# Performance work log

Hardware: AMD Instinct MI355X
Metric: run time of the kernel (lower is better)

The kernel has to match this reference:

```python
import jax, jax.numpy as jnp
import numpy as np

D_MODEL = 1024
N_HEADS = 16
D_HEAD = D_MODEL // N_HEADS


def setup_inputs() -> dict:
    key = jax.random.key(0)
    k_x, k_wqkv, k_bqkv, k_wout, k_bout = jax.random.split(key, 5)
    x = jax.random.normal(k_x, (4, 2048, D_MODEL), dtype=jnp.float32)
    s = 1.0 / np.sqrt(D_MODEL)
    W_qkv = jax.random.uniform(k_wqkv, (D_MODEL, 3 * D_MODEL), jnp.float32, -s, s)
    b_qkv = jax.random.uniform(k_bqkv, (3 * D_MODEL,), jnp.float32, -s, s)
    W_out = jax.random.uniform(k_wout, (D_MODEL, D_MODEL), jnp.float32, -s, s)
    b_out = jax.random.uniform(k_bout, (D_MODEL,), jnp.float32, -s, s)
    return {"x": x, "W_qkv": W_qkv, "b_qkv": b_qkv, "W_out": W_out, "b_out": b_out}


def reference(x, W_qkv, b_qkv, W_out, b_out):
    B, S, _ = x.shape
    qkv = x @ W_qkv + b_qkv                      # [B,S,3*d_model]
    qkv = qkv.reshape(B, S, N_HEADS, 3 * D_HEAD).transpose(0, 2, 1, 3)  # [B,H,S,3*dh]
    q, k, v = jnp.split(qkv, 3, axis=-1)          # each [B,H,S,dh]
    scale = 1.0 / jnp.sqrt(jnp.asarray(D_HEAD, x.dtype))
    scores = jnp.einsum("bhqd,bhkd->bhqk", q, k) * scale  # [B,H,S,S]
    attn_weights = jax.nn.softmax(scores, axis=-1)
    attn = jnp.einsum("bhqk,bhkd->bhqd", attn_weights, v)  # [B,H,S,dh]
    attn = attn.transpose(0, 2, 1, 3).reshape(B, S, D_MODEL)
    return attn @ W_out + b_out
```

## Files before the change

kernel.cpp:

```cpp
#include <hip/hip_runtime.h>

typedef unsigned short u16;
typedef __bf16 bf16x8 __attribute__((ext_vector_type(8)));
typedef __bf16 bf16x4 __attribute__((ext_vector_type(4)));
typedef short s16x4 __attribute__((ext_vector_type(4)));
typedef float f32x4 __attribute__((ext_vector_type(4)));

union U4B8 { uint4 u; bf16x8 v; u16 s[8]; };
union U2S4 { uint2 u2; s16x4 s; bf16x4 h; };

__device__ __forceinline__ u16 f2b(float f) {
  union { float f; unsigned u; } x; x.f = f;
  unsigned u = x.u + 0x7fffu + ((x.u >> 16) & 1u);
  return (u16)(u >> 16);
}

__global__ __launch_bounds__(256) void cvt_f32_bf16(const float* __restrict__ in,
                                                    u16* __restrict__ out) {
  int i = blockIdx.x * 256 + threadIdx.x;
  float4 v = ((const float4*)in)[i];
  ushort4 h;
  h.x = f2b(v.x); h.y = f2b(v.y); h.z = f2b(v.z); h.w = f2b(v.w);
  ((ushort4*)out)[i] = h;
}

__global__ __launch_bounds__(256) void transpose_w(const float* __restrict__ in,
                                                   u16* __restrict__ out, int K, int N) {
  __shared__ u16 t[64 * 72];
  int k0 = blockIdx.y * 64, n0 = blockIdx.x * 64;
  int tid = threadIdx.x;
#pragma unroll
  for (int p = 0; p < 4; ++p) {
    int idx = p * 256 + tid;
    int k = idx >> 4, ng = idx & 15;
    float4 v = *(const float4*)(in + (k0 + k) * N + n0 + ng * 4);
    t[(ng * 4 + 0) * 72 + k] = f2b(v.x);
    t[(ng * 4 + 1) * 72 + k] = f2b(v.y);
    t[(ng * 4 + 2) * 72 + k] = f2b(v.z);
    t[(ng * 4 + 3) * 72 + k] = f2b(v.w);
  }
  __syncthreads();
#pragma unroll
  for (int p = 0; p < 2; ++p) {
    int idx = p * 256 + tid;
    int n = idx >> 3, kg = (idx & 7) * 8;
    uint4 u = *(uint4*)(&t[n * 72 + kg]);
    *(uint4*)(out + (n0 + n) * K + k0 + kg) = u;
  }
}

template <int MODE>
__global__ __launch_bounds__(256) void gemm_bf16(const u16* __restrict__ A,
                                                 const u16* __restrict__ B,
                                                 const float* __restrict__ bias,
                                                 float* __restrict__ outf,
                                                 u16* __restrict__ Qo, u16* __restrict__ Ko,
                                                 u16* __restrict__ Vo) {
  __shared__ u16 a_lds[128 * 32];
  __shared__ u16 b_lds[128 * 32];
  int tid = threadIdx.x;
  int l = tid & 63, w = tid >> 6;
  int wr = (w >> 1) * 64, wc = (w & 1) * 64;
  int m0 = blockIdx.y * 128, n0 = blockIdx.x * 128;
  int r15 = l & 15;
  int ka = (l >> 4) * 8;
  int r0 = tid >> 2, kg0 = (tid & 3) * 8;
  f32x4 acc[4][4] = {};
  for (int kt = 0; kt < 32; ++kt) {
    int k0 = kt * 32;
    __syncthreads();
    __builtin_amdgcn_global_load_lds(
        (const __attribute__((address_space(1))) void*)(A + (m0 + r0) * 1024 + k0 + kg0),
        (__attribute__((address_space(3))) void*)(&a_lds[tid * 8]), 16, 0, 0);
    __builtin_amdgcn_global_load_lds(
        (const __attribute__((address_space(1))) void*)(A + (m0 + 64 + r0) * 1024 + k0 + kg0),
        (__attribute__((address_space(3))) void*)(&a_lds[2048 + tid * 8]), 16, 0, 0);
    __builtin_amdgcn_global_load_lds(
        (const __attribute__((address_space(1))) void*)(B + (n0 + r0) * 1024 + k0 + kg0),
        (__attribute__((address_space(3))) void*)(&b_lds[tid * 8]), 16, 0, 0);
    __builtin_amdgcn_global_load_lds(
        (const __attribute__((address_space(1))) void*)(B + (n0 + 64 + r0) * 1024 + k0 + kg0),
        (__attribute__((address_space(3))) void*)(&b_lds[2048 + tid * 8]), 16, 0, 0);
    __syncthreads();
    bf16x8 af[4], bf[4];
#pragma unroll
    for (int i = 0; i < 4; ++i) {
      U4B8 ua; ua.u = *(uint4*)(&a_lds[(wr + i * 16 + r15) * 32 + ka]); af[i] = ua.v;
      U4B8 ub; ub.u = *(uint4*)(&b_lds[(wc + i * 16 + r15) * 32 + ka]); bf[i] = ub.v;
    }
#pragma unroll
    for (int i = 0; i < 4; ++i)
#pragma unroll
      for (int j = 0; j < 4; ++j)
        acc[i][j] = __builtin_amdgcn_mfma_f32_16x16x32_bf16(af[i], bf[j], acc[i][j], 0, 0, 0);
  }
  int rbase = (l >> 4) * 4;
#pragma unroll
  for (int i = 0; i < 4; ++i)
#pragma unroll
    for (int j = 0; j < 4; ++j) {
      int n = n0 + wc + j * 16 + r15;
      float bv = bias[n];
#pragma unroll
      for (int r = 0; r < 4; ++r) {
        int m = m0 + wr + i * 16 + rbase + r;
        float val = acc[i][j][r] + bv;
        if (MODE == 0) {
          int h = n / 192, rem = n % 192;
          int part = rem >> 6, d = rem & 63;
          int b = m >> 11, s = m & 2047;
          int off = (((b * 16 + h) * 2048) + s) * 64 + d;
          u16 hv = f2b(part == 0 ? val * 0.180336880111f : val);
          if (part == 0) Qo[off] = hv;
          else if (part == 1) Ko[off] = hv;
          else Vo[off] = hv;
        } else {
          outf[m * 1024 + n] = val;
        }
      }
    }
}

__global__ __launch_bounds__(512, 2) void attn_fwd(const u16* __restrict__ Q,
                                                   const u16* __restrict__ K,
                                                   const u16* __restrict__ V,
                                                   u16* __restrict__ O) {
  __shared__ u16 lds[16384];
  int tid = threadIdx.x;
  int l = tid & 63, w = tid >> 6;
  int g = l >> 4, r15 = l & 15, r7 = r15 & 7;
  int bid = blockIdx.x;
  int qb = (bid >> 3) & 7;
  int bh = (bid & 7) * 8 + (bid >> 6);
  const u16* Kb = K + bh * 131072;
  const u16* Vb = V + bh * 131072;
  int ka = g * 8;
  int qbase = qb * 256 + w * 32;
  U4B8 t0, t1, t2, t3;
  t0.u = *(const uint4*)(Q + bh * 131072 + (qbase + r15) * 64 + ka);
  t1.u = *(const uint4*)(Q + bh * 131072 + (qbase + r15) * 64 + 32 + ka);
  t2.u = *(const uint4*)(Q + bh * 131072 + (qbase + 16 + r15) * 64 + ka);
  t3.u = *(const uint4*)(Q + bh * 131072 + (qbase + 16 + r15) * 64 + 32 + ka);
  bf16x8 qf00 = t0.v, qf01 = t1.v, qf10 = t2.v, qf11 = t3.v;

  int kaddr[4];
#pragma unroll
  for (int c = 0; c < 4; ++c) kaddr[c] = (c * 16 + r15) * 64 + ((g ^ r7) << 3);
  int vaddr0[4];
#pragma unroll
  for (int dq = 0; dq < 4; ++dq) {
    int d = r15 + 16 * dq;
    int vsw = ((d >> 3) ^ d) & 15;
    vaddr0[dq] = 8192 + d * 64 + ((g ^ vsw) << 2);
  }

  int krow0 = tid >> 3;
  int kcg = (((tid & 7) ^ (krow0 & 7)) << 3);
  int sr0 = tid >> 3, sdg = (tid & 7) * 8;
  int vwa[8];
#pragma unroll
  for (int i = 0; i < 8; ++i) {
    int d = sdg + i;
    int sw = ((d >> 3) ^ d) & 15;
    vwa[i] = 8192 + d * 64 + ((((sr0 >> 2)) ^ sw) << 2) + (sr0 & 3);
  }
  U4B8 vreg;

#define STAGE(OFFW, TN)                                                                    \
  {                                                                                        \
    int kv0 = (TN) * 64;                                                                   \
    __builtin_amdgcn_global_load_lds(                                                      \
        (const __attribute__((address_space(1))) void*)(Kb + (kv0 + krow0) * 64 + kcg),    \
        (__attribute__((address_space(3))) void*)(&lds[(OFFW) + tid * 8]), 16, 0, 0);      \
    vreg.u = *(const uint4*)(Vb + (kv0 + sr0) * 64 + sdg);                                 \
  }

#define WRITEV(OFFW)                                                                       \
  {                                                                                        \
    _Pragma("unroll") for (int i = 0; i < 8; ++i) {                                        \
      lds[(OFFW) + vwa[i]] = vreg.s[i];                                                    \
    }                                                                                      \
  }

  float l0 = 0.f, l1 = 0.f;
  f32x4 o0[4] = {}, o1[4] = {};

#define COMPUTE(OFFR)                                                                      \
  {                                                                                        \
    _Pragma("unroll") for (int c = 0; c < 4; ++c) {                                        \
      U4B8 k0, k1;                                                                         \
      k0.u = *(const uint4*)(&lds[(OFFR) + kaddr[c]]);                                     \
      k1.u = *(const uint4*)(&lds[(OFFR) + (kaddr[c] ^ 32)]);                              \
      f32x4 z0 = {}, z1 = {};                                                              \
      z0 = __builtin_amdgcn_mfma_f32_16x16x32_bf16(k0.v, qf00, z0, 0, 0, 0);               \
      z0 = __builtin_amdgcn_mfma_f32_16x16x32_bf16(k1.v, qf01, z0, 0, 0, 0);               \
      z1 = __builtin_amdgcn_mfma_f32_16x16x32_bf16(k0.v, qf10, z1, 0, 0, 0);               \
      z1 = __builtin_amdgcn_mfma_f32_16x16x32_bf16(k1.v, qf11, z1, 0, 0, 0);               \
      float a0 = __builtin_amdgcn_exp2f(z0[0]), a1 = __builtin_amdgcn_exp2f(z0[1]);        \
      float a2 = __builtin_amdgcn_exp2f(z0[2]), a3 = __builtin_amdgcn_exp2f(z0[3]);        \
      l0 += (a0 + a1) + (a2 + a3);                                                         \
      U2S4 pa0;                                                                            \
      pa0.h[0] = (__bf16)a0; pa0.h[1] = (__bf16)a1;                                        \
      pa0.h[2] = (__bf16)a2; pa0.h[3] = (__bf16)a3;                                        \
      float b0 = __builtin_amdgcn_exp2f(z1[0]), b1 = __builtin_amdgcn_exp2f(z1[1]);        \
      float b2 = __builtin_amdgcn_exp2f(z1[2]), b3 = __builtin_amdgcn_exp2f(z1[3]);        \
      l1 += (b0 + b1) + (b2 + b3);                                                         \
      U2S4 pa1;                                                                            \
      pa1.h[0] = (__bf16)b0; pa1.h[1] = (__bf16)b1;                                        \
      pa1.h[2] = (__bf16)b2; pa1.h[3] = (__bf16)b3;                                        \
      _Pragma("unroll") for (int dq = 0; dq < 4; ++dq) {                                   \
        U2S4 vb;                                                                           \
        vb.u2 = *(const uint2*)(&lds[(OFFR) + (vaddr0[dq] ^ (16 * c))]);                   \
        o0[dq] = __builtin_amdgcn_mfma_f32_16x16x16bf16_1k(pa0.s, vb.s, o0[dq], 0, 0, 0);  \
        o1[dq] = __builtin_amdgcn_mfma_f32_16x16x16bf16_1k(pa1.s, vb.s, o1[dq], 0, 0, 0);  \
      }                                                                                    \
    }                                                                                      \
  }

  STAGE(0, 0);
  WRITEV(0);
#pragma unroll 1
  for (int tt = 0; tt < 16; ++tt) {
    __syncthreads();
    STAGE(4096, 2 * tt + 1);
    COMPUTE(0);
    WRITEV(4096);
    __syncthreads();
    if (tt < 15) STAGE(0, 2 * tt + 2);
    COMPUTE(4096);
    if (tt < 15) WRITEV(0);
  }
#undef STAGE
#undef WRITEV
#undef COMPUTE

  l0 += __shfl_xor(l0, 16); l0 += __shfl_xor(l0, 32);
  l1 += __shfl_xor(l1, 16); l1 += __shfl_xor(l1, 32);
  float i0 = 1.f / l0, i1 = 1.f / l1;
  float c0[4], c1[4];
#pragma unroll
  for (int j = 0; j < 4; ++j) {
    c0[j] = __shfl(i0, 4 * g + j);
    c1[j] = __shfl(i1, 4 * g + j);
  }
  __syncthreads();
  u16* stg = lds + w * 2048;
#pragma unroll
  for (int j = 0; j < 4; ++j) {
    int rr0 = 4 * g + j;
    int rr1 = 16 + 4 * g + j;
#pragma unroll
    for (int dq = 0; dq < 4; ++dq) {
      int pc = ((dq ^ g) << 4) + r15;
      stg[rr0 * 64 + pc] = f2b(o0[dq][j] * c0[j]);
      stg[rr1 * 64 + pc] = f2b(o1[dq][j] * c1[j]);
    }
  }
  int b = bh >> 4, h = bh & 15;
  int colpair = (l & 31) * 2;
  int rowsel = l >> 5;
#pragma unroll
  for (int it = 0; it < 16; ++it) {
    int rr = 2 * it + rowsel;
    int phys = rr * 64 + (((colpair >> 4) ^ ((rr >> 2) & 3)) << 4) + (colpair & 15);
    unsigned pv = *(const unsigned*)(&stg[phys]);
    int row = qbase + rr;
    *(unsigned*)(&O[(b * 2048 + row) * 1024 + h * 64 + colpair]) = pv;
  }
}

extern "C" void kernel_launch(void* const* d_in, const int* in_sizes, int n_in,
                              void* d_out, int out_size, void* d_ws, size_t ws_size,
                              hipStream_t stream) {
  const float* x = (const float*)d_in[0];
  const float* Wqkv = (const float*)d_in[1];
  const float* bqkv = (const float*)d_in[2];
  const float* Wout = (const float*)d_in[3];
  const float* bout = (const float*)d_in[4];
  float* out = (float*)d_out;

  u16* ws = (u16*)d_ws;
  u16* WtQ = ws;
  u16* WtO = WtQ + 3072 * 1024;
  u16* Xb  = WtO + 1024 * 1024;
  u16* Qw  = Xb + 8192 * 1024;
  u16* Kw  = Qw + 64 * 2048 * 64;
  u16* Vw  = Kw + 64 * 2048 * 64;
  u16* Aw  = Vw + 64 * 2048 * 64;

  cvt_f32_bf16<<<8192, 256, 0, stream>>>(x, Xb);
  transpose_w<<<dim3(48, 16), 256, 0, stream>>>(Wqkv, WtQ, 1024, 3072);
  transpose_w<<<dim3(16, 16), 256, 0, stream>>>(Wout, WtO, 1024, 1024);
  gemm_bf16<0><<<dim3(24, 64), 256, 0, stream>>>(Xb, WtQ, bqkv, nullptr, Qw, Kw, Vw);
  attn_fwd<<<512, 512, 0, stream>>>(Qw, Kw, Vw, Aw);
  gemm_bf16<1><<<dim3(8, 64), 256, 0, stream>>>(Aw, WtO, bout, out, nullptr, nullptr, nullptr);
}
```

Measured before the change: 212.5 us.

## Triple-buffer GEMM LDS loads and merge prep kernels into one launch

The bf16 GEMM now uses three LDS buffers and prefetches the next K-tile with global_load_lds while computing the current one. A vmcnt wait plus a single barrier replaces the two __syncthreads per iteration. The x conversion and both weight transposes are also combined into one launch to cut launch overhead. The trade is more LDS per block (48KB), which could lower occupancy, and correctness relies on the manual waitcnt and barrier ordering.

```diff
diff --git a/kernel.cpp b/kernel.cpp
--- a/kernel.cpp
+++ b/kernel.cpp
@@ -15,20 +15,30 @@
   return (u16)(u >> 16);
 }
 
-__global__ __launch_bounds__(256) void cvt_f32_bf16(const float* __restrict__ in,
-                                                    u16* __restrict__ out) {
-  int i = blockIdx.x * 256 + threadIdx.x;
-  float4 v = ((const float4*)in)[i];
-  ushort4 h;
-  h.x = f2b(v.x); h.y = f2b(v.y); h.z = f2b(v.z); h.w = f2b(v.w);
-  ((ushort4*)out)[i] = h;
-}
-
-__global__ __launch_bounds__(256) void transpose_w(const float* __restrict__ in,
-                                                   u16* __restrict__ out, int K, int N) {
+__global__ __launch_bounds__(256) void prep(const float* __restrict__ x,
+                                            const float* __restrict__ Wqkv,
+                                            const float* __restrict__ Wout,
+                                            u16* __restrict__ Xb,
+                                            u16* __restrict__ WtQ,
+                                            u16* __restrict__ WtO) {
   __shared__ u16 t[64 * 72];
-  int k0 = blockIdx.y * 64, n0 = blockIdx.x * 64;
+  int bid = blockIdx.x;
   int tid = threadIdx.x;
+  if (bid < 8192) {
+    int i = bid * 256 + tid;
+    float4 v = ((const float4*)x)[i];
+    ushort4 h;
+    h.x = f2b(v.x); h.y = f2b(v.y); h.z = f2b(v.z); h.w = f2b(v.w);
+    ((ushort4*)Xb)[i] = h;
+    return;
+  }
+  const float* in; u16* out; int N, bx, by;
+  if (bid < 8960) {
+    int tt = bid - 8192; bx = tt % 48; by = tt / 48; in = Wqkv; out = WtQ; N = 3072;
+  } else {
+    int tt = bid - 8960; bx = tt & 15; by = tt >> 4; in = Wout; out = WtO; N = 1024;
+  }
+  int k0 = by * 64, n0 = bx * 64;
 #pragma unroll
   for (int p = 0; p < 4; ++p) {
     int idx = p * 256 + tid;
@@ -45,7 +55,7 @@
     int idx = p * 256 + tid;
     int n = idx >> 3, kg = (idx & 7) * 8;
     uint4 u = *(uint4*)(&t[n * 72 + kg]);
-    *(uint4*)(out + (n0 + n) * K + k0 + kg) = u;
+    *(uint4*)(out + (n0 + n) * 1024 + k0 + kg) = u;
   }
 }
 
@@ -56,8 +66,8 @@
                                                  float* __restrict__ outf,
                                                  u16* __restrict__ Qo, u16* __restrict__ Ko,
                                                  u16* __restrict__ Vo) {
-  __shared__ u16 a_lds[128 * 32];
-  __shared__ u16 b_lds[128 * 32];
+  __shared__ u16 a_lds[3 * 4096];
+  __shared__ u16 b_lds[3 * 4096];
   int tid = threadIdx.x;
   int l = tid & 63, w = tid >> 6;
   int wr = (w >> 1) * 64, wc = (w & 1) * 64;
@@ -66,34 +76,53 @@
   int ka = (l >> 4) * 8;
   int r0 = tid >> 2, kg0 = (tid & 3) * 8;
   f32x4 acc[4][4] = {};
+
+#define STAGE_G(BUF, KT)                                                                     \
+  {                                                                                          \
+    int kk = (KT) * 32;                                                                      \
+    __builtin_amdgcn_global_load_lds(                                                        \
+        (const __attribute__((address_space(1))) void*)(A + (m0 + r0) * 1024 + kk + kg0),    \
+        (__attribute__((address_space(3))) void*)(&a_lds[(BUF) * 4096 + tid * 8]), 16, 0, 0);\
+    __builtin_amdgcn_global_load_lds(                                                        \
+        (const __attribute__((address_space(1))) void*)(A + (m0 + 64 + r0) * 1024 + kk + kg0),\
+        (__attribute__((address_space(3))) void*)(&a_lds[(BUF) * 4096 + 2048 + tid * 8]), 16, 0, 0);\
+    __builtin_amdgcn_global_load_lds(                                                        \
+        (const __attribute__((address_space(1))) void*)(B + (n0 + r0) * 1024 + kk + kg0),    \
+        (__attribute__((address_space(3))) void*)(&b_lds[(BUF) * 4096 + tid * 8]), 16, 0, 0);\
+    __builtin_amdgcn_global_load_lds(                                                        \
+        (const __attribute__((address_space(1))) void*)(B + (n0 + 64 + r0) * 1024 + kk + kg0),\
+        (__attribute__((address_space(3))) void*)(&b_lds[(BUF) * 4096 + 2048 + tid * 8]), 16, 0, 0);\
+  }
+
+  STAGE_G(0, 0);
+  int cur = 0;
+#pragma unroll 1
   for (int kt = 0; kt < 32; ++kt) {
-    int k0 = kt * 32;
-    __syncthreads();
-    __builtin_amdgcn_global_load_lds(
-        (const __attribute__((address_space(1))) void*)(A + (m0 + r0) * 1024 + k0 + kg0),
-        (__attribute__((address_space(3))) void*)(&a_lds[tid * 8]), 16, 0, 0);
-    __builtin_amdgcn_global_load_lds(
-        (const __attribute__((address_space(1))) void*)(A + (m0 + 64 + r0) * 1024 + k0 + kg0),
-        (__attribute__((address_space(3))) void*)(&a_lds[2048 + tid * 8]), 16, 0, 0);
-    __builtin_amdgcn_global_load_lds(
-        (const __attribute__((address_space(1))) void*)(B + (n0 + r0) * 1024 + k0 + kg0),
-        (__attribute__((address_space(3))) void*)(&b_lds[tid * 8]), 16, 0, 0);
-    __builtin_amdgcn_global_load_lds(
-        (const __attribute__((address_space(1))) void*)(B + (n0 + 64 + r0) * 1024 + k0 + kg0),
-        (__attribute__((address_space(3))) void*)(&b_lds[2048 + tid * 8]), 16, 0, 0);
-    __syncthreads();
+    int nxt = (cur == 2) ? 0 : cur + 1;
+    if (kt < 31) {
+      STAGE_G(nxt, kt + 1);
+      asm volatile("s_waitcnt vmcnt(4)" ::: "memory");
+    } else {
+      asm volatile("s_waitcnt vmcnt(0)" ::: "memory");
+    }
+    __builtin_amdgcn_s_barrier();
+    __builtin_amdgcn_sched_barrier(0);
+    int bo = cur * 4096;
     bf16x8 af[4], bf[4];
 #pragma unroll
     for (int i = 0; i < 4; ++i) {
-      U4B8 ua; ua.u = *(uint4*)(&a_lds[(wr + i * 16 + r15) * 32 + ka]); af[i] = ua.v;
-      U4B8 ub; ub.u = *(uint4*)(&b_lds[(wc + i * 16 + r15) * 32 + ka]); bf[i] = ub.v;
+      U4B8 ua; ua.u = *(uint4*)(&a_lds[bo + (wr + i * 16 + r15) * 32 + ka]); af[i] = ua.v;
+      U4B8 ub; ub.u = *(uint4*)(&b_lds[bo + (wc + i * 16 + r15) * 32 + ka]); bf[i] = ub.v;
     }
 #pragma unroll
     for (int i = 0; i < 4; ++i)
 #pragma unroll
       for (int j = 0; j < 4; ++j)
         acc[i][j] = __builtin_amdgcn_mfma_f32_16x16x32_bf16(af[i], bf[j], acc[i][j], 0, 0, 0);
-  }
+    cur = nxt;
+  }
+#undef STAGE_G
+
   int rbase = (l >> 4) * 4;
 #pragma unroll
   for (int i = 0; i < 4; ++i)
@@ -288,9 +317,7 @@
   u16* Vw  = Kw + 64 * 2048 * 64;
   u16* Aw  = Vw + 64 * 2048 * 64;
 
-  cvt_f32_bf16<<<8192, 256, 0, stream>>>(x, Xb);
-  transpose_w<<<dim3(48, 16), 256, 0, stream>>>(Wqkv, WtQ, 1024, 3072);
-  transpose_w<<<dim3(16, 16), 256, 0, stream>>>(Wout, WtO, 1024, 1024);
+  prep<<<9216, 256, 0, stream>>>(x, Wqkv, Wout, Xb, WtQ, WtO);
   gemm_bf16<0><<<dim3(24, 64), 256, 0, stream>>>(Xb, WtQ, bqkv, nullptr, Qw, Kw, Vw);
   attn_fwd<<<512, 512, 0, stream>>>(Qw, Kw, Vw, Aw);
   gemm_bf16<1><<<dim3(8, 64), 256, 0, stream>>>(Aw, WtO, bout, out, nullptr, nullptr, nullptr);
```

Result: no change. 208.8 us (-1.8%).
